# Kernel tuning notes

Measured on AMD Instinct MI355X. Metric: run time of the kernel, lower is better.

Reference implementation:

```python
import jax, jax.numpy as jnp
import numpy as np
from jax import lax

P = 3            # patch_size
H = W = 32       # spatial size forced by reshape to (32,32)
RATES = (1, 2, 4, 8)
DN = ('NCHW', 'OIHW', 'NCHW')


def setup_inputs() -> dict:
    key = jax.random.key(0)
    k0, k1, k2, k3 = jax.random.split(key, 4)
    foreground = jax.random.normal(k0, (8, 256, H, W), jnp.float32)
    background = jax.random.normal(k1, (8, 256, H, W), jnp.float32)
    mask = (jax.random.uniform(k2, (1, 1, H, W)) < 0.5).astype(jnp.float32)  # binary hole mask
    conv_w = jax.random.normal(k3, (4, 64, 256, 3, 3), jnp.float32) * 0.02
    conv_b = jnp.zeros((4, 64), jnp.float32)
    return {"foreground": foreground, "mask": mask, "background": background,
            "conv_w": conv_w, "conv_b": conv_b}


def _extract_patches(x):
    # x: [C, H+2, W+2] (padded) -> [H*W, C, 3, 3], patch index = h*W + w (torch unfold order)
    C = x.shape[0]
    cols = jnp.stack([x[:, i:i + H, j:j + W] for i in range(P) for j in range(P)], axis=0)  # [9,C,H,W]
    return cols.reshape(P, P, C, H, W).transpose(3, 4, 2, 0, 1).reshape(H * W, C, P, P)


def _forward(foreground, mask, background, conv_w, conv_b):
    bg = background * (1.0 - mask)
    bg_p = jnp.pad(bg, ((0, 0), (0, 0), (1, 1), (1, 1)))
    # per-sample patch kernels, L2-normalized (cosine similarity)
    kernels = jax.vmap(_extract_patches)(bg_p) + 1e-7          # [bz, L=1024, C, 3, 3]
    norm = jnp.sqrt(jnp.sum(kernels ** 2, axis=(2, 3, 4), keepdims=True))
    kernels = kernels / norm

    def corr(fm, kern):  # fm [C,H,W], kern [L,C,3,3] -> [L,H,W]
        return lax.conv_general_dilated(fm[None], kern, (1, 1), 'SAME', dimension_numbers=DN)[0]

    scores = jax.vmap(corr)(foreground, kernels)               # [bz, L, H, W]
    # propagation: depthwise 3x3 ones conv (groups=L, padding=1) == windowed sum
    scores = lax.reduce_window(scores, jnp.float32(0), lax.add,
                               (1, 1, 3, 3), (1, 1, 1, 1), 'SAME')
    attn = jax.nn.softmax(scores, axis=1)                      # softmax over the L patch axis

    def tconv(a, kern):
        # conv_transpose2d(a, kern[in=L,out=C], padding=1) == conv2d with spatially
        # flipped kernels and in/out swapped, padding = 3-1-1 = 1 (SAME)
        wct = jnp.flip(kern, axis=(2, 3)).transpose(1, 0, 2, 3)  # [C, L, 3, 3]
        return lax.conv_general_dilated(a[None], wct, (1, 1), 'SAME', dimension_numbers=DN)[0]

    recovered = jax.vmap(tconv)(attn, kernels)                 # [bz, C, H, W]
    recovered = recovered * mask / (P * P)
    final = recovered + foreground * (1.0 - mask)

    outs = []
    for g in range(4):  # 4 fused dilated conv branches (structurally distinct weights)
        r = RATES[g]
        o = lax.conv_general_dilated(final, conv_w[g], (1, 1), [(r, r), (r, r)],
                                     rhs_dilation=(r, r), dimension_numbers=DN)
        outs.append(jax.nn.relu(o + conv_b[g][None, :, None, None]))
    return jnp.concatenate(outs, axis=1)                       # [bz, 256, H, W]


def reference(foreground, mask, background, conv_w, conv_b):
    return _forward(foreground, mask, background, conv_w, conv_b)
```

## Files before the change

kernel.cpp:

```cpp
#include <hip/hip_runtime.h>

typedef __attribute__((ext_vector_type(8))) short short8;
typedef __attribute__((ext_vector_type(4))) float f32x4;
typedef __attribute__((ext_vector_type(4))) unsigned int uint4v;

#define HW 32
#define L 1024
#define C_IN 256
#define BATCH 8
#define NQ 1156

static __device__ __forceinline__ unsigned short f2bf(float f){
  unsigned int u = __float_as_uint(f);
  unsigned int r = (u + 0x7FFFu + ((u >> 16) & 1u)) >> 16;
  return (unsigned short)r;
}
static __device__ __forceinline__ float bf2f(unsigned short h){
  return __uint_as_float(((unsigned int)h) << 16);
}

#define GLDS16(g, l) __builtin_amdgcn_global_load_lds(                          \
    (const __attribute__((address_space(1))) void*)(g),                         \
    (__attribute__((address_space(3))) void*)(l), 16, 0, 0)

__global__ __launch_bounds__(256) void fused_prep(const float* __restrict__ fg,
                                                  const float* __restrict__ bgd,
                                                  const float* __restrict__ mask,
                                                  unsigned short* __restrict__ fgT,
                                                  unsigned short* __restrict__ mbgT,
                                                  unsigned short* __restrict__ mbgS,
                                                  float* __restrict__ psum,
                                                  const float* __restrict__ conv_w,
                                                  unsigned short* __restrict__ Wr,
                                                  unsigned short* __restrict__ zpage){
  __shared__ float T[64][65];
  int blk = blockIdx.x;
  if (blk >= 512){
    if (blk == 512) zpage[threadIdx.x] = 0;
    int idx = (blk - 512) * 256 + threadIdx.x;
    int c = idx & 255;
    int rest = idx >> 8;
    int n = rest & 63;
    int sg = rest >> 6;
    int s = sg % 9, g = sg / 9;
    Wr[idx] = f2bf(conv_w[(((size_t)(g * 64 + n)) * C_IN + c) * 9 + s]);
    return;
  }
  const int NP = BATCH * L;
  int bx = blk & 15, cb = (blk >> 4) & 3, b = blk >> 6;
  int p0 = bx * 64, c0 = cb * 64;
  int tid = threadIdx.x;
  int rr = tid >> 4, px = (tid & 15) * 4;
  int cx = tid & 15, ppb = tid >> 4;
  const float* F = fg  + ((size_t)b * C_IN + c0) * L + p0;
  const float* G = bgd + ((size_t)b * C_IN + c0) * L + p0;

  #pragma unroll
  for (int it = 0; it < 4; it++){
    int cc = it * 16 + rr;
    float4 v = *(const float4*)(F + (size_t)cc * L + px);
    T[cc][px] = v.x; T[cc][px + 1] = v.y; T[cc][px + 2] = v.z; T[cc][px + 3] = v.w;
  }
  __syncthreads();
  #pragma unroll
  for (int it = 0; it < 4; it++){
    int pp = it * 16 + ppb;
    float t0 = T[cx * 4][pp], t1 = T[cx * 4 + 1][pp], t2 = T[cx * 4 + 2][pp], t3 = T[cx * 4 + 3][pp];
    ushort4 o; o.x = f2bf(t0); o.y = f2bf(t1); o.z = f2bf(t2); o.w = f2bf(t3);
    *(ushort4*)&fgT[(size_t)(b * L + p0 + pp) * C_IN + c0 + cx * 4] = o;
    float s = t0 + t1 + t2 + t3;
    #pragma unroll
    for (int off = 8; off; off >>= 1) s += __shfl_xor(s, off, 16);
    if (cx == 0) psum[(size_t)(cb * 3 + 0) * NP + b * L + p0 + pp] = s;
  }
  __syncthreads();

  float4 mv = *(const float4*)(mask + p0 + px);
  mv.x = 1.f - mv.x; mv.y = 1.f - mv.y; mv.z = 1.f - mv.z; mv.w = 1.f - mv.w;
  #pragma unroll
  for (int it = 0; it < 4; it++){
    int cc = it * 16 + rr;
    float4 v = *(const float4*)(G + (size_t)cc * L + px);
    v.x *= mv.x; v.y *= mv.y; v.z *= mv.z; v.w *= mv.w;
    T[cc][px] = v.x; T[cc][px + 1] = v.y; T[cc][px + 2] = v.z; T[cc][px + 3] = v.w;
    ushort4 o; o.x = f2bf(v.x); o.y = f2bf(v.y); o.z = f2bf(v.z); o.w = f2bf(v.w);
    *(ushort4*)&mbgS[((size_t)b * C_IN + c0 + cc) * L + p0 + px] = o;
  }
  __syncthreads();
  #pragma unroll
  for (int it = 0; it < 4; it++){
    int pp = it * 16 + ppb;
    float t0 = T[cx * 4][pp], t1 = T[cx * 4 + 1][pp], t2 = T[cx * 4 + 2][pp], t3 = T[cx * 4 + 3][pp];
    ushort4 o; o.x = f2bf(t0); o.y = f2bf(t1); o.z = f2bf(t2); o.w = f2bf(t3);
    *(ushort4*)&mbgT[(size_t)(b * L + p0 + pp) * C_IN + c0 + cx * 4] = o;
    float s1 = t0 + t1 + t2 + t3;
    float s2 = t0 * t0 + t1 * t1 + t2 * t2 + t3 * t3;
    #pragma unroll
    for (int off = 8; off; off >>= 1){
      s1 += __shfl_xor(s1, off, 16);
      s2 += __shfl_xor(s2, off, 16);
    }
    if (cx == 0){
      psum[(size_t)(cb * 3 + 1) * NP + b * L + p0 + pp] = s1;
      psum[(size_t)(cb * 3 + 2) * NP + b * L + p0 + pp] = s2;
    }
  }
}

__global__ __launch_bounds__(512) void gemm_d_rn(const unsigned short* __restrict__ fgT,
                                                 const unsigned short* __restrict__ mbgT,
                                                 unsigned short* __restrict__ D,
                                                 const float* __restrict__ psum,
                                                 float* __restrict__ rn,
                                                 float* __restrict__ eps){
  __shared__ unsigned short As[64][256];
  __shared__ unsigned short Bs[64][256];
  int bid = blockIdx.x;
  if (bid >= 2048){
    int idx = (bid - 2048) * 512 + threadIdx.x;
    int b = idx >> 10, l = idx & 1023;
    int ly = l >> 5, lx = l & 31;
    const int NP = BATCH * L;
    float n2 = 2.304e-11f;
    #pragma unroll
    for (int s = 0; s < 9; s++){
      int y = ly + s / 3 - 1, x = lx + s % 3 - 1;
      if ((unsigned)y < HW && (unsigned)x < HW){
        int q = b * L + y * HW + x;
        float s1 = 0.f, s2 = 0.f;
        #pragma unroll
        for (int k = 0; k < 4; k++){
          s1 += psum[(size_t)(k * 3 + 1) * NP + q];
          s2 += psum[(size_t)(k * 3 + 2) * NP + q];
        }
        n2 += s2 + 2e-7f * s1;
      }
    }
    rn[idx] = 1.f / sqrtf(n2);
    float ev = 0.f;
    const int tw[5] = {1, 2, 3, 2, 1};
    #pragma unroll
    for (int oy = -2; oy <= 2; oy++)
      #pragma unroll
      for (int ox = -2; ox <= 2; ox++){
        int y = ly + oy, x = lx + ox;
        if ((unsigned)y < HW && (unsigned)x < HW){
          int q = b * L + y * HW + x;
          float s0 = 0.f;
          #pragma unroll
          for (int k = 0; k < 4; k++) s0 += psum[(size_t)(k * 3 + 0) * NP + q];
          ev += (float)(tw[oy + 2] * tw[ox + 2]) * s0;
        }
      }
    eps[idx] = 1e-7f * ev;
    return;
  }
  int b = bid & 7, r = bid >> 3;
  int by = r >> 4, bx = r & 15;
  const unsigned short* Ab = fgT  + ((size_t)b * L + by * 64) * C_IN;
  const unsigned short* Bb = mbgT + ((size_t)b * L + bx * 64) * C_IN;
  int tid = threadIdx.x, lane = tid & 63, wv = tid >> 6;
  int row_off = lane >> 5, slot = lane & 31;
  int q = slot >> 3, sl = slot & 7;
  #pragma unroll
  for (int i = 0; i < 4; i++){
    int rr = wv * 8 + i * 2 + row_off;
    int srcs = q * 8 + (sl ^ (rr & 7));
    GLDS16(Ab + (size_t)rr * C_IN + srcs * 8, &As[wv * 8 + i * 2][0]);
    GLDS16(Bb + (size_t)rr * C_IN + srcs * 8, &Bs[wv * 8 + i * 2][0]);
  }
  __syncthreads();
  int wm = (wv & 1) * 32, wn = (wv >> 1) * 16;
  int rsel = lane & 15, sx = lane >> 4;
  f32x4 acc[2] = {};
  #pragma unroll
  for (int st = 0; st < 8; st++){
    int gs = st * 4 + sx, qq = gs >> 3, ss = gs & 7;
    short8 af[2], bf;
    #pragma unroll
    for (int i = 0; i < 2; i++){
      int ra = wm + i * 16 + rsel;
      af[i] = *(const short8*)&As[ra][(qq * 8 + (ss ^ (ra & 7))) * 8];
    }
    int rb = wn + rsel;
    bf = *(const short8*)&Bs[rb][(qq * 8 + (ss ^ (rb & 7))) * 8];
    #pragma unroll
    for (int i = 0; i < 2; i++)
      acc[i] = __builtin_amdgcn_mfma_f32_16x16x32_bf16(af[i], bf, acc[i], 0, 0, 0);
  }
  unsigned short* Db = D + ((size_t)b << 20);
  int rowb = (lane >> 4) * 4, col = lane & 15;
  #pragma unroll
  for (int i = 0; i < 2; i++)
    #pragma unroll
    for (int r2 = 0; r2 < 4; r2++)
      Db[(size_t)(by * 64 + wm + i * 16 + rowb + r2) * L + bx * 64 + wn + col] = f2bf(acc[i][r2]);
}

__global__ __launch_bounds__(256) void box3(const unsigned short* __restrict__ D,
                                            unsigned short* __restrict__ W){
  int bid = blockIdx.x;
  int b = bid & 7;
  int q2 = (bid >> 3) * 2 + (threadIdx.x >> 7);
  int v0 = (threadIdx.x & 127) * 8;
  int qy = q2 / 34 - 1, qx = q2 % 34 - 1;
  const unsigned short* Db = D + ((size_t)b << 20);
  float a[8] = {0.f, 0.f, 0.f, 0.f, 0.f, 0.f, 0.f, 0.f};
  #pragma unroll
  for (int dy = -1; dy <= 1; dy++)
    #pragma unroll
    for (int dx = -1; dx <= 1; dx++){
      int y = qy + dy, x = qx + dx;
      if ((unsigned)y < HW && (unsigned)x < HW){
        uint4v v = *(const uint4v*)(Db + ((size_t)(y * HW + x) << 10) + v0);
        #pragma unroll
        for (int j = 0; j < 4; j++){
          a[j * 2]     += __uint_as_float(v[j] << 16);
          a[j * 2 + 1] += __uint_as_float(v[j] & 0xffff0000u);
        }
      }
    }
  uint4v o;
  #pragma unroll
  for (int j = 0; j < 4; j++)
    o[j] = (unsigned)f2bf(a[j * 2]) | ((unsigned)f2bf(a[j * 2 + 1]) << 16);
  *(uint4v*)(W + ((size_t)(b * NQ + q2) << 10) + v0) = o;
}

static __device__ __forceinline__ unsigned tap2(const unsigned* __restrict__ row32,
                                                int idx, int sh){
  int a0 = idx & ~1;
  unsigned q0 = row32[a0 >> 1];
  if (sh == 0) return q0;
  unsigned q1 = row32[((a0 + 2) & 1023) >> 1];
  return (q0 >> 16) | (q1 << 16);
}

__global__ __launch_bounds__(512) void prop_softmax_diag(const unsigned short* __restrict__ W,
                                                         const float* __restrict__ eps,
                                                         const float* __restrict__ rn,
                                                         unsigned short* __restrict__ AR){
  __shared__ __align__(16) unsigned short Wl[16][1024];
  __shared__ float redm[8][4], reds[8][4];
  int bid = blockIdx.x;
  int b = bid & 7, tile = bid >> 3;
  int py0 = (tile >> 4) * 2, px0 = (tile & 15) * 2;
  const unsigned short* Wb = W + (size_t)b * NQ * L;
  int tid = threadIdx.x, lane = tid & 63, wv = tid >> 6;
  #pragma unroll
  for (int k = 0; k < 4; k++){
    int u = k * 8 + wv;
    int rr = u >> 1, half = u & 1;
    int qs = (py0 + (rr >> 2)) * 34 + (px0 + (rr & 3));
    GLDS16(Wb + (((size_t)qs) << 10) + half * 512 + lane * 8, &Wl[rr][half * 512]);
  }
  int l0 = tid * 2;
  int ly = l0 >> 5, lx0 = l0 & 31;
  float2 rnl = *(const float2*)&rn[b * L + l0];
  float ev[4];
  #pragma unroll
  for (int o = 0; o < 4; o++)
    ev[o] = eps[b * L + (py0 + (o >> 1)) * HW + (px0 + (o & 1))];
  __syncthreads();
  float val[4][2];
  #pragma unroll
  for (int o = 0; o < 4; o++){
    int oy = o >> 1, ox = o & 1;
    float a0 = 0.f, a1 = 0.f;
    #pragma unroll
    for (int s = 0; s < 9; s++){
      const int dy = s / 3 - 1, dx = s % 3 - 1;
      const int dlt = dy * 32 + dx;
      const int sh = dx & 1;
      bool rok = (unsigned)(ly + dy) < HW;
      int idx = (l0 + dlt) & 1023;
      unsigned ov = tap2((const unsigned*)&Wl[(oy + dy + 1) * 4 + (ox + dx + 1)][0], idx, sh);
      float f0 = __uint_as_float(ov << 16), f1 = __uint_as_float(ov & 0xffff0000u);
      a0 += (rok && (unsigned)(lx0 + 0 + dx) < HW) ? f0 : 0.f;
      a1 += (rok && (unsigned)(lx0 + 1 + dx) < HW) ? f1 : 0.f;
    }
    val[o][0] = rnl.x * (a0 + ev[o]); val[o][1] = rnl.y * (a1 + ev[o]);
  }
  #pragma unroll
  for (int o = 0; o < 4; o++){
    float m = fmaxf(val[o][0], val[o][1]);
    #pragma unroll
    for (int off = 32; off; off >>= 1) m = fmaxf(m, __shfl_xor(m, off));
    if (lane == 0) redm[wv][o] = m;
  }
  __syncthreads();
  float mf[4];
  #pragma unroll
  for (int o = 0; o < 4; o++){
    float m = redm[0][o];
    #pragma unroll
    for (int w = 1; w < 8; w++) m = fmaxf(m, redm[w][o]);
    mf[o] = m;
  }
  float e[4][2];
  #pragma unroll
  for (int o = 0; o < 4; o++){
    e[o][0] = __expf(val[o][0] - mf[o]);
    e[o][1] = __expf(val[o][1] - mf[o]);
    float t = e[o][0] + e[o][1];
    #pragma unroll
    for (int off = 32; off; off >>= 1) t += __shfl_xor(t, off);
    if (lane == 0) reds[wv][o] = t;
  }
  __syncthreads();
  #pragma unroll
  for (int o = 0; o < 4; o++){
    float t = reds[0][o];
    #pragma unroll
    for (int w = 1; w < 8; w++) t += reds[w][o];
    float inv = 1.f / t;
    int p = (py0 + (o >> 1)) * HW + (px0 + (o & 1));
    unsigned short* O = AR + ((size_t)b << 20) + ((size_t)p << 10);
    ushort2 ov;
    ov.x = f2bf(e[o][0] * inv * rnl.x); ov.y = f2bf(e[o][1] * inv * rnl.y);
    *(ushort2*)&O[l0] = ov;
  }
}

__global__ __launch_bounds__(512) void u_stencil(const unsigned short* __restrict__ AR,
                                                 unsigned short* __restrict__ U){
  __shared__ __align__(16) unsigned short Al[16][1024];
  int bid = blockIdx.x;
  int b = bid & 7, tile = bid >> 3;
  int py0 = (tile >> 4) * 2, px0 = (tile & 15) * 2;
  int tid = threadIdx.x, lane = tid & 63, wv = tid >> 6;
  const unsigned short* A = AR + ((size_t)b << 20);
  #pragma unroll
  for (int k = 0; k < 4; k++){
    int u = k * 8 + wv;
    int rr = u >> 1, half = u & 1;
    int yy = py0 + (rr >> 2) - 1, xx = px0 + (rr & 3) - 1;
    bool rok = ((unsigned)yy < HW) && ((unsigned)xx < HW);
    int p2 = rok ? (yy * HW + xx) : 0;
    GLDS16(A + (((size_t)p2) << 10) + half * 512 + lane * 8, &Al[rr][half * 512]);
  }
  int vmask = 0;
  #pragma unroll
  for (int rr = 0; rr < 16; rr++){
    int yy = py0 + (rr >> 2) - 1, xx = px0 + (rr & 3) - 1;
    if (((unsigned)yy < HW) && ((unsigned)xx < HW)) vmask |= 1 << rr;
  }
  __syncthreads();
  int v0 = tid * 2;
  int vy = v0 >> 5, vx0 = v0 & 31;
  #pragma unroll
  for (int o = 0; o < 4; o++){
    int oy = o >> 1, ox = o & 1;
    float a0 = 0.f, a1 = 0.f;
    #pragma unroll
    for (int s = 0; s < 9; s++){
      const int dy = s / 3 - 1, dx = s % 3 - 1;
      const int dlt = dy * 32 + dx;
      const int sh = dx & 1;
      const int rr = (oy + dy + 1) * 4 + (ox + dx + 1);
      bool rok = ((vmask >> rr) & 1) && ((unsigned)(vy + dy) < HW);
      int idx = (v0 + dlt) & 1023;
      unsigned ov = tap2((const unsigned*)&Al[rr][0], idx, sh);
      float f0 = __uint_as_float(ov << 16), f1 = __uint_as_float(ov & 0xffff0000u);
      a0 += (rok && (unsigned)(vx0 + 0 + dx) < HW) ? f0 : 0.f;
      a1 += (rok && (unsigned)(vx0 + 1 + dx) < HW) ? f1 : 0.f;
    }
    int p = (py0 + oy) * HW + (px0 + ox);
    unsigned short* O = U + ((size_t)b << 20) + ((size_t)p << 10);
    ushort2 ov2;
    ov2.x = f2bf(a0); ov2.y = f2bf(a1);
    *(ushort2*)&O[v0] = ov2;
  }
}

__global__ __launch_bounds__(512) void gemm3_final(const unsigned short* __restrict__ U,
                                                   const unsigned short* __restrict__ mbgS,
                                                   const float* __restrict__ mask,
                                                   const unsigned short* __restrict__ fgT,
                                                   unsigned short* __restrict__ finalT){
  __shared__ unsigned short As[2][64][64];
  __shared__ unsigned short Bs[2][64][64];
  int bid = blockIdx.x;
  int b = bid & 7, r = bid >> 3;
  int mt = r >> 2, ct = r & 3;
  int tid = threadIdx.x, lane = tid & 63, wv = tid >> 6;
  int wm = (wv & 1) * 32, wn = (wv >> 1) * 16;
  int rsel = lane & 15;
  int srow = lane >> 3, scol = ((lane & 7) ^ srow) * 8;
  const unsigned short* Ab = U    + ((size_t)b * L + mt * 64) * L;
  const unsigned short* Bb = mbgS + ((size_t)b * C_IN + ct * 64) * L;
  GLDS16(Ab + (size_t)(wv * 8 + srow) * L + scol, &As[0][wv * 8][0]);
  GLDS16(Bb + (size_t)(wv * 8 + srow) * L + scol, &Bs[0][wv * 8][0]);
  __syncthreads();
  f32x4 acc[2] = {};
  int cur = 0;
  for (int t = 0; t < 16; ++t){
    short8 af[2][2], bf[2];
    #pragma unroll
    for (int kk = 0; kk < 2; kk++){
      int s0 = kk * 4 + (lane >> 4);
      int col = ((s0 ^ (rsel & 7)) << 3);
      #pragma unroll
      for (int i = 0; i < 2; i++)
        af[kk][i] = *(const short8*)&As[cur][wm + i * 16 + rsel][col];
      bf[kk] = *(const short8*)&Bs[cur][wn + rsel][col];
    }
    if (t + 1 < 16){
      int nb = cur ^ 1;
      size_t kt = (size_t)(t + 1) * 64;
      GLDS16(Ab + (size_t)(wv * 8 + srow) * L + kt + scol, &As[nb][wv * 8][0]);
      GLDS16(Bb + (size_t)(wv * 8 + srow) * L + kt + scol, &Bs[nb][wv * 8][0]);
    }
    #pragma unroll
    for (int kk = 0; kk < 2; kk++)
      #pragma unroll
      for (int i = 0; i < 2; i++)
        acc[i] = __builtin_amdgcn_mfma_f32_16x16x32_bf16(af[kk][i], bf[kk], acc[i], 0, 0, 0);
    __syncthreads();
    cur ^= 1;
  }
  int rowb = (lane >> 4) * 4, col = lane & 15;
  #pragma unroll
  for (int i = 0; i < 2; i++)
    #pragma unroll
    for (int r2 = 0; r2 < 4; r2++){
      int p = mt * 64 + wm + i * 16 + rowb + r2;
      int c = ct * 64 + wn + col;
      unsigned short o;
      if (mask[p] != 0.f) o = f2bf(acc[i][r2] * (1.f / 9.f));
      else                o = fgT[((size_t)b * L + p) * C_IN + c];
      finalT[((size_t)b * L + p) * C_IN + c] = o;
    }
}

__global__ __launch_bounds__(512) void branch_gemm(const unsigned short* __restrict__ finalT,
                                                   const unsigned short* __restrict__ Wr,
                                                   const float* __restrict__ conv_b,
                                                   const unsigned short* __restrict__ zpage,
                                                   float* __restrict__ out){
  __shared__ unsigned short As[2][64][64];
  __shared__ unsigned short Bs[2][64][64];
  int nwg = gridDim.x, bid = blockIdx.x;
  int nid = (bid & 7) * (nwg >> 3) + (bid >> 3);
  int bg = nid >> 4, pt = nid & 15;
  int b = bg >> 2, g = bg & 3;
  int rate = 1 << g;
  int p0 = pt * 64;
  int tid = threadIdx.x, lane = tid & 63, wv = tid >> 6;
  int wm = (wv & 1) * 32, wn = (wv >> 1) * 16;
  int rsel = lane & 15;
  int srow = lane >> 3;
  int scol = ((lane & 7) ^ srow) * 8;
  const unsigned short* FT = finalT + (size_t)b * L * C_IN;
  const unsigned short* WG = Wr + (size_t)(g * 9) * 64 * C_IN;

  int prow = p0 + wv * 8 + srow;
  int ayy = prow >> 5, axx = prow & 31;
  auto a_src = [&](int t) -> const unsigned short* {
    int s = t >> 2, q = t & 3;
    int dy = s / 3 - 1, dx = s - (s / 3) * 3 - 1;
    int iy = ayy + rate * dy, ix = axx + rate * dx;
    if ((unsigned)iy < HW && (unsigned)ix < HW)
      return FT + (size_t)(iy * HW + ix) * C_IN + q * 64 + scol;
    return zpage;
  };
  auto b_src = [&](int t) -> const unsigned short* {
    int s = t >> 2, q = t & 3;
    int n = wv * 8 + srow;
    return WG + (size_t)(s * 64 + n) * C_IN + q * 64 + scol;
  };

  f32x4 acc[2] = {};
  GLDS16(a_src(0), &As[0][wv * 8][0]);
  GLDS16(b_src(0), &Bs[0][wv * 8][0]);
  __syncthreads();
  int cur = 0;
  for (int t = 0; t < 36; ++t){
    short8 af[2][2], bf[2];
    #pragma unroll
    for (int kk = 0; kk < 2; kk++){
      int s0 = kk * 4 + (lane >> 4);
      int col = ((s0 ^ (rsel & 7)) << 3);
      #pragma unroll
      for (int i = 0; i < 2; i++)
        af[kk][i] = *(const short8*)&As[cur][wm + i * 16 + rsel][col];
      bf[kk] = *(const short8*)&Bs[cur][wn + rsel][col];
    }
    if (t + 1 < 36){
      int nb = cur ^ 1;
      GLDS16(a_src(t + 1), &As[nb][wv * 8][0]);
      GLDS16(b_src(t + 1), &Bs[nb][wv * 8][0]);
    }
    #pragma unroll
    for (int kk = 0; kk < 2; kk++)
      #pragma unroll
      for (int i = 0; i < 2; i++)
        acc[i] = __builtin_amdgcn_mfma_f32_16x16x32_bf16(af[kk][i], bf[kk], acc[i], 0, 0, 0);
    __syncthreads();
    cur ^= 1;
  }
  int rowb = (lane >> 4) * 4, col = lane & 15;
  float* O = out + (size_t)(b * 256 + g * 64) * L;
  int n = wn + col;
  float bias = conv_b[g * 64 + n];
  #pragma unroll
  for (int i = 0; i < 2; i++)
    #pragma unroll
    for (int r2 = 0; r2 < 4; r2++){
      int p = p0 + wm + i * 16 + rowb + r2;
      O[(size_t)n * L + p] = fmaxf(acc[i][r2] + bias, 0.f);
    }
}


extern "C" void kernel_launch(void* const* d_in, const int* in_sizes, int n_in,
                              void* d_out, int out_size, void* d_ws, size_t ws_size,
                              hipStream_t stream){
  const float* fg     = (const float*)d_in[0];
  const float* mask   = (const float*)d_in[1];
  const float* bgd    = (const float*)d_in[2];
  const float* conv_w = (const float*)d_in[3];
  const float* conv_b = (const float*)d_in[4];

  char* ws = (char*)d_ws;
  unsigned short* D      = (unsigned short*)(ws + 0);
  unsigned short* W      = (unsigned short*)(ws + 16777216);
  unsigned short* AR     = (unsigned short*)(ws + 35717120);
  unsigned short* U      = (unsigned short*)(ws + 52494336);
  unsigned short* mbgT   = (unsigned short*)(ws + 69271552);
  unsigned short* mbgS   = (unsigned short*)(ws + 73465856);
  unsigned short* finalT = (unsigned short*)(ws + 77660160);
  unsigned short* Wr     = (unsigned short*)(ws + 81854464);
  float*          psum   = (float*)(ws + 83034112);
  float*          rn     = (float*)(ws + 83427328);
  float*          eps    = (float*)(ws + 83460096);
  unsigned short* zpage  = (unsigned short*)(ws + 83492864);
  unsigned short* fgT    = (unsigned short*)d_out;
  float* out = (float*)d_out;

  fused_prep<<<2816, 256, 0, stream>>>(fg, bgd, mask, fgT, mbgT, mbgS, psum,
                                       conv_w, Wr, zpage);
  gemm_d_rn<<<2064, 512, 0, stream>>>(fgT, mbgT, D, psum, rn, eps);
  box3<<<4624, 256, 0, stream>>>(D, W);
  prop_softmax_diag<<<2048, 512, 0, stream>>>(W, eps, rn, AR);
  u_stencil<<<2048, 512, 0, stream>>>(AR, U);
  gemm3_final<<<512, 512, 0, stream>>>(U, mbgS, mask, fgT, finalT);
  branch_gemm<<<512, 512, 0, stream>>>(finalT, Wr, conv_b, zpage, out);
}
```

Before: 108.8 us.

## Store W and AR rows in zero-padded 34x34 layout to drop stencil bounds checks

The intermediate W and AR buffers now store each 1024-wide L vector as a zero-bordered 34x34 grid (stride 1184) instead of a dense 32x32 row. box3 and prop_softmax_diag write the zero borders, so the 3x3 stencil loops in prop_softmax_diag and u_stencil read neighbors directly without per-tap bounds masks or wraparound logic. The cost is about 16% more memory traffic and LDS per row, an extra partial global-to-LDS load per row, and extra border-zeroing stores.

Measured after the change: 112.2 us. 1.03x slower.

```diff
diff --git a/kernel.cpp b/kernel.cpp
--- a/kernel.cpp
+++ b/kernel.cpp
@@ -9,6 +9,7 @@
 #define C_IN 256
 #define BATCH 8
 #define NQ 1156
+#define PSTR 1184
 
 static __device__ __forceinline__ unsigned short f2bf(float f){
   unsigned int u = __float_as_uint(f);
@@ -198,7 +199,7 @@
 }
 
 __global__ __launch_bounds__(256) void box3(const unsigned short* __restrict__ D,
-                                            unsigned short* __restrict__ W){
+                                            unsigned short* __restrict__ Wp){
   int bid = blockIdx.x;
   int b = bid & 7;
   int q2 = (bid >> 3) * 2 + (threadIdx.x >> 7);
@@ -220,42 +221,51 @@
         }
       }
     }
-  uint4v o;
-  #pragma unroll
-  for (int j = 0; j < 4; j++)
-    o[j] = (unsigned)f2bf(a[j * 2]) | ((unsigned)f2bf(a[j * 2 + 1]) << 16);
-  *(uint4v*)(W + ((size_t)(b * NQ + q2) << 10) + v0) = o;
+  unsigned short* Wrow = Wp + ((size_t)(b * NQ + q2)) * PSTR;
+  int vp0 = 36 + (v0 >> 5) * 34 + (v0 & 31);
+  #pragma unroll
+  for (int j = 0; j < 4; j++){
+    ushort2 o2; o2.x = f2bf(a[j * 2]); o2.y = f2bf(a[j * 2 + 1]);
+    *(ushort2*)&Wrow[vp0 + 2 * j] = o2;
+  }
+  int k = threadIdx.x & 127;
+  if (k < 80){
+    int pos = (k < 18) ? 2 * k : (k < 49) ? 68 + 34 * (k - 18) : 1122 + 2 * (k - 49);
+    ushort2 z; z.x = 0; z.y = 0;
+    *(ushort2*)&Wrow[pos] = z;
+  }
 }
 
 static __device__ __forceinline__ unsigned tap2(const unsigned* __restrict__ row32,
                                                 int idx, int sh){
-  int a0 = idx & ~1;
-  unsigned q0 = row32[a0 >> 1];
-  if (sh == 0) return q0;
-  unsigned q1 = row32[((a0 + 2) & 1023) >> 1];
+  if (sh == 0) return row32[idx >> 1];
+  unsigned q0 = row32[idx >> 1];
+  unsigned q1 = row32[(idx >> 1) + 1];
   return (q0 >> 16) | (q1 << 16);
 }
 
-__global__ __launch_bounds__(512) void prop_softmax_diag(const unsigned short* __restrict__ W,
+__global__ __launch_bounds__(512) void prop_softmax_diag(const unsigned short* __restrict__ Wp,
                                                          const float* __restrict__ eps,
                                                          const float* __restrict__ rn,
-                                                         unsigned short* __restrict__ AR){
-  __shared__ __align__(16) unsigned short Wl[16][1024];
+                                                         unsigned short* __restrict__ ARp){
+  __shared__ __align__(16) unsigned short Wl[16][PSTR];
   __shared__ float redm[8][4], reds[8][4];
   int bid = blockIdx.x;
   int b = bid & 7, tile = bid >> 3;
   int py0 = (tile >> 4) * 2, px0 = (tile & 15) * 2;
-  const unsigned short* Wb = W + (size_t)b * NQ * L;
+  const unsigned short* Wb = Wp + (size_t)b * NQ * PSTR;
   int tid = threadIdx.x, lane = tid & 63, wv = tid >> 6;
   #pragma unroll
-  for (int k = 0; k < 4; k++){
+  for (int k = 0; k < 6; k++){
     int u = k * 8 + wv;
-    int rr = u >> 1, half = u & 1;
+    int rr = u / 3, part = u - rr * 3;
     int qs = (py0 + (rr >> 2)) * 34 + (px0 + (rr & 3));
-    GLDS16(Wb + (((size_t)qs) << 10) + half * 512 + lane * 8, &Wl[rr][half * 512]);
+    const unsigned short* src = Wb + (size_t)qs * PSTR + part * 512 + lane * 8;
+    if (part < 2) GLDS16(src, &Wl[rr][part * 512]);
+    else if (lane < 20) GLDS16(src, &Wl[rr][1024]);
   }
   int l0 = tid * 2;
-  int ly = l0 >> 5, lx0 = l0 & 31;
+  int lp = 36 + (l0 >> 5) * 34 + (l0 & 31);
   float2 rnl = *(const float2*)&rn[b * L + l0];
   float ev[4];
   #pragma unroll
@@ -270,14 +280,10 @@
     #pragma unroll
     for (int s = 0; s < 9; s++){
       const int dy = s / 3 - 1, dx = s % 3 - 1;
-      const int dlt = dy * 32 + dx;
-      const int sh = dx & 1;
-      bool rok = (unsigned)(ly + dy) < HW;
-      int idx = (l0 + dlt) & 1023;
-      unsigned ov = tap2((const unsigned*)&Wl[(oy + dy + 1) * 4 + (ox + dx + 1)][0], idx, sh);
-      float f0 = __uint_as_float(ov << 16), f1 = __uint_as_float(ov & 0xffff0000u);
-      a0 += (rok && (unsigned)(lx0 + 0 + dx) < HW) ? f0 : 0.f;
-      a1 += (rok && (unsigned)(lx0 + 1 + dx) < HW) ? f1 : 0.f;
+      unsigned ov = tap2((const unsigned*)&Wl[(oy + dy + 1) * 4 + (ox + dx + 1)][0],
+                         lp + dy * 34 + dx, dx & 1);
+      a0 += __uint_as_float(ov << 16);
+      a1 += __uint_as_float(ov & 0xffff0000u);
     }
     val[o][0] = rnl.x * (a0 + ev[o]); val[o][1] = rnl.y * (a1 + ev[o]);
   }
@@ -308,6 +314,7 @@
     if (lane == 0) reds[wv][o] = t;
   }
   __syncthreads();
+  unsigned short* Ob = ARp + (size_t)b * L * PSTR;
   #pragma unroll
   for (int o = 0; o < 4; o++){
     float t = reds[0][o];
@@ -315,39 +322,46 @@
     for (int w = 1; w < 8; w++) t += reds[w][o];
     float inv = 1.f / t;
     int p = (py0 + (o >> 1)) * HW + (px0 + (o & 1));
-    unsigned short* O = AR + ((size_t)b << 20) + ((size_t)p << 10);
     ushort2 ov;
     ov.x = f2bf(e[o][0] * inv * rnl.x); ov.y = f2bf(e[o][1] * inv * rnl.y);
-    *(ushort2*)&O[l0] = ov;
-  }
-}
-
-__global__ __launch_bounds__(512) void u_stencil(const unsigned short* __restrict__ AR,
+    *(ushort2*)&Ob[(size_t)p * PSTR + lp] = ov;
+  }
+  int brow = tid >> 7, k = tid & 127;
+  if (k < 80){
+    int pos = (k < 18) ? 2 * k : (k < 49) ? 68 + 34 * (k - 18) : 1122 + 2 * (k - 49);
+    int pz = (py0 + (brow >> 1)) * HW + (px0 + (brow & 1));
+    ushort2 z; z.x = 0; z.y = 0;
+    *(ushort2*)&Ob[(size_t)pz * PSTR + pos] = z;
+  }
+}
+
+__global__ __launch_bounds__(512) void u_stencil(const unsigned short* __restrict__ ARp,
                                                  unsigned short* __restrict__ U){
-  __shared__ __align__(16) unsigned short Al[16][1024];
+  __shared__ __align__(16) unsigned short Al[16][PSTR];
   int bid = blockIdx.x;
   int b = bid & 7, tile = bid >> 3;
   int py0 = (tile >> 4) * 2, px0 = (tile & 15) * 2;
   int tid = threadIdx.x, lane = tid & 63, wv = tid >> 6;
-  const unsigned short* A = AR + ((size_t)b << 20);
-  #pragma unroll
-  for (int k = 0; k < 4; k++){
+  const unsigned short* Ab = ARp + (size_t)b * L * PSTR;
+  #pragma unroll
+  for (int k = 0; k < 6; k++){
     int u = k * 8 + wv;
-    int rr = u >> 1, half = u & 1;
+    int rr = u / 3, part = u - rr * 3;
     int yy = py0 + (rr >> 2) - 1, xx = px0 + (rr & 3) - 1;
     bool rok = ((unsigned)yy < HW) && ((unsigned)xx < HW);
-    int p2 = rok ? (yy * HW + xx) : 0;
-    GLDS16(A + (((size_t)p2) << 10) + half * 512 + lane * 8, &Al[rr][half * 512]);
-  }
-  int vmask = 0;
-  #pragma unroll
-  for (int rr = 0; rr < 16; rr++){
-    int yy = py0 + (rr >> 2) - 1, xx = px0 + (rr & 3) - 1;
-    if (((unsigned)yy < HW) && ((unsigned)xx < HW)) vmask |= 1 << rr;
+    if (rok){
+      const unsigned short* src = Ab + (size_t)(yy * HW + xx) * PSTR + part * 512 + lane * 8;
+      if (part < 2) GLDS16(src, &Al[rr][part * 512]);
+      else if (lane < 20) GLDS16(src, &Al[rr][1024]);
+    } else {
+      unsigned* dst = (unsigned*)&Al[rr][part * 512];
+      if (part < 2){ dst[lane] = 0; dst[lane + 64] = 0; dst[lane + 128] = 0; dst[lane + 192] = 0; }
+      else if (lane < 40){ dst[lane] = 0; dst[lane + 40] = 0; }
+    }
   }
   __syncthreads();
   int v0 = tid * 2;
-  int vy = v0 >> 5, vx0 = v0 & 31;
+  int vp = 36 + (v0 >> 5) * 34 + (v0 & 31);
   #pragma unroll
   for (int o = 0; o < 4; o++){
     int oy = o >> 1, ox = o & 1;
@@ -355,15 +369,10 @@
     #pragma unroll
     for (int s = 0; s < 9; s++){
       const int dy = s / 3 - 1, dx = s % 3 - 1;
-      const int dlt = dy * 32 + dx;
-      const int sh = dx & 1;
-      const int rr = (oy + dy + 1) * 4 + (ox + dx + 1);
-      bool rok = ((vmask >> rr) & 1) && ((unsigned)(vy + dy) < HW);
-      int idx = (v0 + dlt) & 1023;
-      unsigned ov = tap2((const unsigned*)&Al[rr][0], idx, sh);
-      float f0 = __uint_as_float(ov << 16), f1 = __uint_as_float(ov & 0xffff0000u);
-      a0 += (rok && (unsigned)(vx0 + 0 + dx) < HW) ? f0 : 0.f;
-      a1 += (rok && (unsigned)(vx0 + 1 + dx) < HW) ? f1 : 0.f;
+      unsigned ov = tap2((const unsigned*)&Al[(oy + dy + 1) * 4 + (ox + dx + 1)][0],
+                         vp + dy * 34 + dx, dx & 1);
+      a0 += __uint_as_float(ov << 16);
+      a1 += __uint_as_float(ov & 0xffff0000u);
     }
     int p = (py0 + oy) * HW + (px0 + ox);
     unsigned short* O = U + ((size_t)b << 20) + ((size_t)p << 10);
@@ -524,26 +533,26 @@
 
   char* ws = (char*)d_ws;
   unsigned short* D      = (unsigned short*)(ws + 0);
-  unsigned short* W      = (unsigned short*)(ws + 16777216);
-  unsigned short* AR     = (unsigned short*)(ws + 35717120);
-  unsigned short* U      = (unsigned short*)(ws + 52494336);
-  unsigned short* mbgT   = (unsigned short*)(ws + 69271552);
-  unsigned short* mbgS   = (unsigned short*)(ws + 73465856);
-  unsigned short* finalT = (unsigned short*)(ws + 77660160);
-  unsigned short* Wr     = (unsigned short*)(ws + 81854464);
-  float*          psum   = (float*)(ws + 83034112);
-  float*          rn     = (float*)(ws + 83427328);
-  float*          eps    = (float*)(ws + 83460096);
-  unsigned short* zpage  = (unsigned short*)(ws + 83492864);
+  unsigned short* Wp     = (unsigned short*)(ws + 16777216);
+  unsigned short* ARp    = (unsigned short*)(ws + 38674432);
+  unsigned short* U      = (unsigned short*)(ws + 58073088);
+  unsigned short* mbgT   = (unsigned short*)(ws + 74850304);
+  unsigned short* mbgS   = (unsigned short*)(ws + 79044608);
+  unsigned short* finalT = (unsigned short*)(ws + 83238912);
+  unsigned short* Wr     = (unsigned short*)(ws + 87433216);
+  float*          psum   = (float*)(ws + 88612864);
+  float*          rn     = (float*)(ws + 89006080);
+  float*          eps    = (float*)(ws + 89038848);
+  unsigned short* zpage  = (unsigned short*)(ws + 89071616);
   unsigned short* fgT    = (unsigned short*)d_out;
   float* out = (float*)d_out;
 
   fused_prep<<<2816, 256, 0, stream>>>(fg, bgd, mask, fgT, mbgT, mbgS, psum,
                                        conv_w, Wr, zpage);
   gemm_d_rn<<<2064, 512, 0, stream>>>(fgT, mbgT, D, psum, rn, eps);
-  box3<<<4624, 256, 0, stream>>>(D, W);
-  prop_softmax_diag<<<2048, 512, 0, stream>>>(W, eps, rn, AR);
-  u_stencil<<<2048, 512, 0, stream>>>(AR, U);
+  box3<<<4624, 256, 0, stream>>>(D, Wp);
+  prop_softmax_diag<<<2048, 512, 0, stream>>>(Wp, eps, rn, ARp);
+  u_stencil<<<2048, 512, 0, stream>>>(ARp, U);
   gemm3_final<<<512, 512, 0, stream>>>(U, mbgS, mask, fgT, finalT);
   branch_gemm<<<512, 512, 0, stream>>>(finalT, Wr, conv_b, zpage, out);
 }
```
